# Kernel optimization log

Hardware: AMD Instinct MI355X
Metric: run time of the kernel (lower is better)

The kernel has to match this reference:

```python
import jax, jax.numpy as jnp
import numpy as np

HIDDEN = 512
EXP = 2048  # hidden * expansion_factor(4)

def _glorot(key, shape):
    fan_in = shape[0]
    return jax.random.normal(key, shape, dtype=jnp.float32) / np.sqrt(fan_in)

def setup_inputs() -> dict:
    key = jax.random.key(0)
    ks = jax.random.split(key, 6)
    B, S = 4, 4096
    return {
        "x": jax.random.normal(ks[0], (B, S, HIDDEN), dtype=jnp.float32),
        "W_in1": _glorot(ks[1], (HIDDEN, EXP)),
        "b_in1": jnp.zeros((EXP,), jnp.float32),
        "W_in2": _glorot(ks[2], (HIDDEN, EXP)),
        "b_in2": jnp.zeros((EXP,), jnp.float32),
        "W_z": _glorot(ks[3], (EXP, EXP)),
        "b_z": jnp.zeros((EXP,), jnp.float32),
        "W_h": _glorot(ks[4], (EXP, EXP)),
        "b_h": jnp.zeros((EXP,), jnp.float32),
        "W_out": _glorot(ks[5], (EXP, HIDDEN)),
        "b_out": jnp.zeros((HIDDEN,), jnp.float32),
    }

def _min_gru(x_in, W_z, b_z, W_h, b_h):
    # minGRU: h_t = (1 - z_t) * h_{t-1} + z_t * h_tilde_t, h_0 = 0
    z = jax.nn.sigmoid(jnp.einsum("bse,ef->bsf", x_in, W_z) + b_z)
    h_tilde = jnp.einsum("bse,ef->bsf", x_in, W_h) + b_h
    a = 1.0 - z          # decay coeff
    b = z * h_tilde      # input term
    def combine(c1, c2):
        a1, b1 = c1
        a2, b2 = c2
        return (a1 * a2, b1 * a2 + b2)
    _, h = jax.lax.associative_scan(combine, (a, b), axis=1)
    return h

def reference(x, W_in1, b_in1, W_in2, b_in2, W_z, b_z, W_h, b_h, W_out, b_out):
    x_in = jax.nn.silu(jnp.einsum("bsd,de->bse", x, W_in1) + b_in1)
    x_skip = jax.nn.silu(jnp.einsum("bsd,de->bse", x, W_in2) + b_in2)
    h = _min_gru(x_in, W_z, b_z, W_h, b_h)
    return jnp.einsum("bse,ed->bsd", x_skip + h, W_out) + b_out
```

## Files before the change

kernel.cpp:

```cpp
#include <hip/hip_runtime.h>
#include <hip/hip_bf16.h>


typedef __bf16 bf16x8 __attribute__((ext_vector_type(8)));
typedef __bf16 bf16x4 __attribute__((ext_vector_type(4)));
typedef float  f32x4  __attribute__((ext_vector_type(4)));

#define DEVINL __device__ __forceinline__

DEVINL void async_ld16(const __bf16* g, __bf16* l) {
    __builtin_amdgcn_global_load_lds(
        (const __attribute__((address_space(1))) void*)g,
        (__attribute__((address_space(3))) void*)l, 16, 0, 0);
}

DEVINL float fsigmoid(float v) { return 1.0f / (1.0f + __expf(-v)); }

template <int MODE>
__global__ __launch_bounds__(512, 4)
void gemm4(const __bf16* __restrict__ A, const __bf16* __restrict__ Bt,
           const float* __restrict__ bias, const float* __restrict__ bias2,
           void* __restrict__ out, void* __restrict__ out2, int N, int K,
           int bps, int seg_stride, int row_off)
{
    struct KL { __bf16 A[128 * 32]; __bf16 B[256 * 32]; };
    __shared__ union SM4 {
        KL kl[2];
        __bf16 ct[64 * 264];
    } sm;
    const int tid = threadIdx.x;
    const int bx = blockIdx.x;
    const int seg = bx / bps;
    const int within = bx - seg * bps;
    const int gm0 = row_off + seg * seg_stride + within * 128;
    const int om0 = bx * 128;
    const int n0 = blockIdx.y * 256;

    const int rA = tid >> 2,         kA = (tid & 3) ^ ((tid >> 3) & 3);
    const int c0 = tid, c1 = tid + 512;
    const int rB0 = c0 >> 2,         kB0 = (c0 & 3) ^ ((c0 >> 3) & 3);
    const int rB1 = c1 >> 2,         kB1 = (c1 & 3) ^ ((c1 >> 3) & 3);
    const __bf16* Ag  = A  + (size_t)(gm0 + rA)  * K + kA  * 8;
    const __bf16* Bg0 = Bt + (size_t)(n0 + rB0) * K + kB0 * 8;
    const __bf16* Bg1 = Bt + (size_t)(n0 + rB1) * K + kB1 * 8;

    const int lane = tid & 63;
    const int wave = tid >> 6;
    const int wm = wave >> 2;
    const int wn = wave & 3;
    const int quad = lane >> 4;
    const int r = lane & 15;
    const int swz = (quad ^ ((r >> 1) & 3)) * 8;

    f32x4 acc[4][4] = {};

    const int T = K >> 5;

    auto stage = [&](int t, int b) {
        const int kt = t << 5;
        async_ld16(Ag  + kt, sm.kl[b].A + tid * 8);
        async_ld16(Bg0 + kt, sm.kl[b].B + c0 * 8);
        async_ld16(Bg1 + kt, sm.kl[b].B + c1 * 8);
    };

    stage(0, 0);

    for (int t = 0; t < T; ++t) {
        const int cur = t & 1;
        if (t + 1 < T) {
            stage(t + 1, cur ^ 1);
            asm volatile("s_waitcnt vmcnt(3)\n\ts_barrier" ::: "memory");
        } else {
            asm volatile("s_waitcnt vmcnt(0)\n\ts_barrier" ::: "memory");
        }

        const __bf16* ap = sm.kl[cur].A + (wm * 64 + r) * 32 + swz;
        const __bf16* bp = sm.kl[cur].B + (wn * 64 + r) * 32 + swz;
        bf16x8 af[4], bf_[4];
#pragma unroll
        for (int m = 0; m < 4; ++m) af[m] = *(const bf16x8*)(ap + m * 512);
#pragma unroll
        for (int n = 0; n < 4; ++n) bf_[n] = *(const bf16x8*)(bp + n * 512);

        __builtin_amdgcn_s_setprio(1);
#pragma unroll
        for (int m = 0; m < 4; ++m)
#pragma unroll
            for (int n = 0; n < 4; ++n)
                acc[m][n] = __builtin_amdgcn_mfma_f32_16x16x32_bf16(
                    af[m], bf_[n], acc[m][n], 0, 0, 0);
        __builtin_amdgcn_s_setprio(0);

        asm volatile("s_waitcnt lgkmcnt(0)\n\ts_barrier" ::: "memory");
    }

    const bool lo = n0 < 2048;
    __bf16* dst = (__bf16*)out;
    const int cb = n0;
    const size_t stride = (size_t)N;
    float bvj[4];
#pragma unroll
    for (int nf = 0; nf < 4; ++nf) {
        const int gc = n0 + wn * 64 + nf * 16 + r;
        bvj[nf] = lo ? bias[gc] : bias2[gc - 2048];
    }

#pragma unroll
    for (int p = 0; p < 2; ++p) {
        if (wm == p) {
#pragma unroll
            for (int mm = 0; mm < 4; ++mm)
#pragma unroll
                for (int nf = 0; nf < 4; ++nf)
#pragma unroll
                    for (int k = 0; k < 4; ++k) {
                        const float v = acc[mm][nf][k] + bvj[nf];
                        sm.ct[(mm * 16 + quad * 4 + k) * 264 +
                              (wn * 64 + nf * 16 + r)] = (__bf16)v;
                    }
        }
        __syncthreads();
#pragma unroll
        for (int q = 0; q < 4; ++q) {
            const int chunk = q * 512 + tid;
            const int trow = chunk >> 5;
            const int tc = (chunk & 31) * 8;
            const bf16x8 vv = *(const bf16x8*)(sm.ct + trow * 264 + tc);
            *(bf16x8*)(dst + (size_t)(om0 + p * 64 + trow) * stride + cb + tc) = vv;
        }
        __syncthreads();
    }
}

struct KLoopSM { __bf16 A[2][128 * 32]; __bf16 B[2][128 * 32]; };

template <int MODE>
__global__ __launch_bounds__(256)
void gemm_bt(const __bf16* __restrict__ A, const __bf16* __restrict__ Bt,
             const float* __restrict__ bias, const float* __restrict__ bias2,
             void* __restrict__ out, void* __restrict__ out2, int N, int K,
             int bps, int seg_stride, int row_off)
{
    __shared__ union SM {
        KLoopSM kl;
        __bf16 ct[64 * 136];
        float  ctf[32 * 132];
    } sm;
    const int tid = threadIdx.x;
    const int bx = blockIdx.x;
    const int by = blockIdx.y;
    const int seg = bx / bps;
    const int within = bx - seg * bps;
    const int gm0 = row_off + seg * seg_stride + within * 128;
    const int om0 = bx * 128;
    const int n0 = by * 128;

    const int c0 = tid, c1 = tid + 256;
    const int r0 = c0 >> 2, k0 = (c0 & 3) ^ ((c0 >> 3) & 3);
    const int r1 = c1 >> 2, k1 = (c1 & 3) ^ ((c1 >> 3) & 3);
    const __bf16* Ag0 = A  + (size_t)(gm0 + r0) * K + k0 * 8;
    const __bf16* Ag1 = A  + (size_t)(gm0 + r1) * K + k1 * 8;
    const __bf16* Bg0 = Bt + (size_t)(n0 + r0) * K + k0 * 8;
    const __bf16* Bg1 = Bt + (size_t)(n0 + r1) * K + k1 * 8;

    const int lane = tid & 63;
    const int wave = tid >> 6;
    const int wrow = (wave >> 1) * 64;
    const int wcol = (wave & 1) * 64;
    const int quad = lane >> 4;
    const int r = lane & 15;
    const int swz = (quad ^ ((r >> 1) & 3)) * 8;

    f32x4 acc[4][4] = {};

    const int T = K >> 5;
    async_ld16(Ag0, sm.kl.A[0] + c0 * 8);
    async_ld16(Ag1, sm.kl.A[0] + c1 * 8);
    async_ld16(Bg0, sm.kl.B[0] + c0 * 8);
    async_ld16(Bg1, sm.kl.B[0] + c1 * 8);

    for (int t = 0; t < T; ++t) {
        const int cur = t & 1;
        if (t + 1 < T) {
            const int kt = (t + 1) << 5;
            async_ld16(Ag0 + kt, sm.kl.A[cur ^ 1] + c0 * 8);
            async_ld16(Ag1 + kt, sm.kl.A[cur ^ 1] + c1 * 8);
            async_ld16(Bg0 + kt, sm.kl.B[cur ^ 1] + c0 * 8);
            async_ld16(Bg1 + kt, sm.kl.B[cur ^ 1] + c1 * 8);
            asm volatile("s_waitcnt vmcnt(4)\n\ts_barrier" ::: "memory");
        } else {
            asm volatile("s_waitcnt vmcnt(0)\n\ts_barrier" ::: "memory");
        }

        const __bf16* ap = sm.kl.A[cur] + (wrow + r) * 32 + swz;
        const __bf16* bp = sm.kl.B[cur] + (wcol + r) * 32 + swz;
        bf16x8 af[4], bf_[4];
#pragma unroll
        for (int i = 0; i < 4; ++i) af[i] = *(const bf16x8*)(ap + i * 512);
#pragma unroll
        for (int i = 0; i < 4; ++i) bf_[i] = *(const bf16x8*)(bp + i * 512);
#pragma unroll
        for (int i = 0; i < 4; ++i)
#pragma unroll
            for (int j = 0; j < 4; ++j)
                acc[i][j] = __builtin_amdgcn_mfma_f32_16x16x32_bf16(
                    af[i], bf_[j], acc[i][j], 0, 0, 0);

        asm volatile("s_waitcnt lgkmcnt(0)\n\ts_barrier" ::: "memory");
    }

    if (MODE == 3) {
        float bvj[4];
#pragma unroll
        for (int j = 0; j < 4; ++j)
            bvj[j] = bias[n0 + wcol + j * 16 + r];
#pragma unroll
        for (int p = 0; p < 4; ++p) {
#pragma unroll
            for (int j = 0; j < 4; ++j)
#pragma unroll
                for (int k = 0; k < 4; ++k)
                    sm.ctf[((wave >> 1) * 16 + quad * 4 + k) * 132 +
                           (wcol + j * 16 + r)] = acc[p][j][k] + bvj[j];
            __syncthreads();
#pragma unroll
            for (int q = 0; q < 4; ++q) {
                const int chunk = q * 256 + tid;
                const int trow = chunk >> 5;
                const int tc4 = (chunk & 31) * 4;
                const f32x4 vv = *(const f32x4*)(sm.ctf + trow * 132 + tc4);
                const int grow = om0 + (trow >> 4) * 64 + p * 16 + (trow & 15);
                *(f32x4*)((float*)out + (size_t)grow * N + n0 + tc4) = vv;
            }
            __syncthreads();
        }
    } else {
        const bool lo = n0 < 2048;
        __bf16* dst;
        int cb;
        size_t stride;
        if (MODE == 0) {
            dst = lo ? (__bf16*)out : (__bf16*)out2;
            cb = lo ? n0 : n0 - 2048;
            stride = 2048;
        } else {
            dst = (__bf16*)out;
            cb = n0;
            stride = (size_t)N;
        }
        float bvj[4];
#pragma unroll
        for (int j = 0; j < 4; ++j) {
            const int gc = n0 + wcol + j * 16 + r;
            bvj[j] = lo ? bias[gc] : bias2[gc - 2048];
        }
#pragma unroll
        for (int p = 0; p < 2; ++p) {
#pragma unroll
            for (int ii = 0; ii < 2; ++ii) {
                const int i = 2 * p + ii;
#pragma unroll
                for (int j = 0; j < 4; ++j)
#pragma unroll
                    for (int k = 0; k < 4; ++k) {
                        const float v = acc[i][j][k] + bvj[j];
                        const __bf16 o = (MODE == 0) ? (__bf16)(v * fsigmoid(v))
                                                     : (__bf16)v;
                        sm.ct[((wave >> 1) * 32 + ii * 16 + quad * 4 + k) * 136 +
                              (wcol + j * 16 + r)] = o;
                    }
            }
            __syncthreads();
#pragma unroll
            for (int q = 0; q < 4; ++q) {
                const int chunk = q * 256 + tid;
                const int trow = chunk >> 4;
                const int tc = (chunk & 15) * 8;
                const bf16x8 vv = *(const bf16x8*)(sm.ct + trow * 136 + tc);
                const int grow = om0 + (trow >> 5) * 64 + p * 32 + (trow & 31);
                *(bf16x8*)(dst + (size_t)grow * stride + cb + tc) = vv;
            }
            __syncthreads();
        }
    }
}

#define SSEG 32
#define SCOLS 32
__global__ __launch_bounds__(1024)
void scan_kernel(const __bf16* __restrict__ raw, __bf16* __restrict__ xskip,
                 float* __restrict__ carry, int CS, int S, int t0, int first)
{
    __shared__ float Als[SSEG][SCOLS];
    __shared__ float Bls[SSEG][SCOLS];
    const int lane = threadIdx.x & (SCOLS - 1);
    const int w = threadIdx.x >> 5;
    const int nb8 = gridDim.x >> 3;
    const int lin = (blockIdx.x & 7) * nb8 + (blockIdx.x >> 3);
    const int gpb = 2048 / SCOLS;
    const int batch = lin / gpb;
    const int col = (lin - batch * gpb) * SCOLS + lane;
    const int L = CS / SSEG;
    const int tbeg = w * L;

    const size_t rbase = ((size_t)batch * CS + tbeg) * 4096 + col;

    float av[32], bv[32];
    float A = 1.0f, Bv = 0.0f;
    {
        size_t idx = rbase;
#pragma unroll
        for (int t = 0; t < 32; ++t, idx += 4096) {
            const float z = fsigmoid((float)raw[idx]);
            const float b = z * (float)raw[idx + 2048];
            const float a = 1.0f - z;
            av[t] = a;
            bv[t] = b;
            Bv = a * Bv + b;
            A *= a;
        }
    }
    Als[w][lane] = A;
    Bls[w][lane] = Bv;
    __syncthreads();

    const int ch = batch * 2048 + col;
    float h = first ? 0.0f : carry[ch];
    for (int s = 0; s < w; ++s)
        h = Als[s][lane] * h + Bls[s][lane];
    if (w == SSEG - 1)
        carry[ch] = A * h + Bv;

    {
        size_t gidx = ((size_t)batch * S + t0 + tbeg) * 2048 + col;
#pragma unroll
        for (int t = 0; t < 32; ++t, gidx += 2048) {
            h = av[t] * h + bv[t];
            xskip[gidx] = (__bf16)((float)xskip[gidx] + h);
        }
    }
}

__global__ __launch_bounds__(256)
void conv_f32_bf16(const float* __restrict__ x, __bf16* __restrict__ y, int n4)
{
    const int i = blockIdx.x * 256 + threadIdx.x;
    if (i >= n4) return;
    const float4 v = ((const float4*)x)[i];
    bf16x4 o;
    o[0] = (__bf16)v.x; o[1] = (__bf16)v.y; o[2] = (__bf16)v.z; o[3] = (__bf16)v.w;
    ((bf16x4*)y)[i] = o;
}

__global__ __launch_bounds__(256)
void transpose_bf16(const float* __restrict__ W, __bf16* __restrict__ Wt, int K, int N)
{
    __shared__ float tile[32][33];
    const int tx = threadIdx.x & 31;
    const int ty = threadIdx.x >> 5;
    const int nb = blockIdx.x * 32;
    const int kb = blockIdx.y * 32;
#pragma unroll
    for (int i = 0; i < 32; i += 8)
        tile[ty + i][tx] = W[(size_t)(kb + ty + i) * N + nb + tx];
    __syncthreads();
#pragma unroll
    for (int i = 0; i < 32; i += 8)
        Wt[(size_t)(nb + ty + i) * K + kb + tx] = (__bf16)tile[tx][ty + i];
}

extern "C" void kernel_launch(void* const* d_in, const int* in_sizes, int n_in,
                              void* d_out, int out_size, void* d_ws, size_t ws_size,
                              hipStream_t stream)
{
    const float* x     = (const float*)d_in[0];
    const float* W_in1 = (const float*)d_in[1];
    const float* b_in1 = (const float*)d_in[2];
    const float* W_in2 = (const float*)d_in[3];
    const float* b_in2 = (const float*)d_in[4];
    const float* W_z   = (const float*)d_in[5];
    const float* b_z   = (const float*)d_in[6];
    const float* W_h   = (const float*)d_in[7];
    const float* b_h   = (const float*)d_in[8];
    const float* W_out = (const float*)d_in[9];
    const float* b_out = (const float*)d_in[10];

    const int B = 4, S = 4096, H = 512, E = 2048;
    const int M = B * S;
    const int CS = 1024;
    const int NC = S / CS;
    const int MC = B * CS;

    const size_t MiB = 1024 * 1024;
    const size_t NEEDED = 183 * MiB;
    if (ws_size < NEEDED) return;

    char* ws = (char*)d_ws;
    __bf16* xb    = (__bf16*)(ws + 0);
    __bf16* rawzh = (__bf16*)(ws + 0);
    float*  carry = (float*) (ws + 32 * MiB);
    __bf16* xin   = (__bf16*)(ws + 33 * MiB);
    __bf16* xskip = (__bf16*)(ws + 97 * MiB);
    __bf16* Wt12  = (__bf16*)(ws + 161 * MiB);
    __bf16* Wtzh  = (__bf16*)(ws + 165 * MiB);
    __bf16* Wto   = (__bf16*)(ws + 181 * MiB);

    conv_f32_bf16<<<(M * H / 4 + 255) / 256, 256, 0, stream>>>(x, xb, M * H / 4);
    transpose_bf16<<<dim3(E / 32, H / 32), 256, 0, stream>>>(W_in1, Wt12, H, E);
    transpose_bf16<<<dim3(E / 32, H / 32), 256, 0, stream>>>(W_in2, Wt12 + (size_t)E * H, H, E);
    transpose_bf16<<<dim3(E / 32, E / 32), 256, 0, stream>>>(W_z, Wtzh, E, E);
    transpose_bf16<<<dim3(E / 32, E / 32), 256, 0, stream>>>(W_h, Wtzh + (size_t)E * E, E, E);
    transpose_bf16<<<dim3(H / 32, E / 32), 256, 0, stream>>>(W_out, Wto, E, H);

    gemm_bt<0><<<dim3(M / 128, 2 * E / 128), 256, 0, stream>>>(
        xb, Wt12, b_in1, b_in2, xin, xskip, 2 * E, H, M / 128, 0, 0);

    for (int c = 0; c < NC; ++c) {
        const int row_off = c * CS;
        gemm4<4><<<dim3(MC / 128, 2 * E / 256), 512, 0, stream>>>(
            xin, Wtzh, b_z, b_h, rawzh, nullptr, 2 * E, E, CS / 128, S, row_off);
        scan_kernel<<<(B * E) / SCOLS, 1024, 0, stream>>>(
            rawzh, xskip, carry, CS, S, row_off, c == 0);
    }

    gemm_bt<3><<<dim3(M / 128, H / 128), 256, 0, stream>>>(
        xskip, Wto, b_out, nullptr, (float*)d_out, nullptr, H, E, M / 128, 0, 0);
}
```

Before: 652.5 us.

## Enlarge z/h GEMM tile to 256x256 with 64-deep K steps

Replaces the 128x256 tile, K=32 z/h projection GEMM with a 256x256 tile that stages 64 K-elements per step. It uses an 8-way XOR swizzle for the wider LDS rows, and each wave now accumulates 8x4 MFMA fragments. This raises arithmetic intensity per LDS load, halves the number of barrier-separated K iterations, and halves the block count. In exchange, LDS use grows to about 128KB for the double buffer, register pressure doubles and occupancy drops to 2 blocks per CU. The chunked grid may also underfill the GPU.

```diff
diff --git a/kernel.cpp b/kernel.cpp
--- a/kernel.cpp
+++ b/kernel.cpp
@@ -17,14 +17,14 @@
 DEVINL float fsigmoid(float v) { return 1.0f / (1.0f + __expf(-v)); }
 
 template <int MODE>
-__global__ __launch_bounds__(512, 4)
-void gemm4(const __bf16* __restrict__ A, const __bf16* __restrict__ Bt,
-           const float* __restrict__ bias, const float* __restrict__ bias2,
-           void* __restrict__ out, void* __restrict__ out2, int N, int K,
-           int bps, int seg_stride, int row_off)
-{
-    struct KL { __bf16 A[128 * 32]; __bf16 B[256 * 32]; };
-    __shared__ union SM4 {
+__global__ __launch_bounds__(512, 2)
+void gemm3k(const __bf16* __restrict__ A, const __bf16* __restrict__ Bt,
+            const float* __restrict__ bias, const float* __restrict__ bias2,
+            void* __restrict__ out, void* __restrict__ out2, int N, int K,
+            int bps, int seg_stride, int row_off)
+{
+    struct KL { __bf16 A[256 * 64]; __bf16 B[256 * 64]; };
+    __shared__ union SM3K {
         KL kl[2];
         __bf16 ct[64 * 264];
     } sm;
@@ -32,17 +32,24 @@
     const int bx = blockIdx.x;
     const int seg = bx / bps;
     const int within = bx - seg * bps;
-    const int gm0 = row_off + seg * seg_stride + within * 128;
-    const int om0 = bx * 128;
+    const int gm0 = row_off + seg * seg_stride + within * 256;
+    const int om0 = bx * 256;
     const int n0 = blockIdx.y * 256;
 
-    const int rA = tid >> 2,         kA = (tid & 3) ^ ((tid >> 3) & 3);
-    const int c0 = tid, c1 = tid + 512;
-    const int rB0 = c0 >> 2,         kB0 = (c0 & 3) ^ ((c0 >> 3) & 3);
-    const int rB1 = c1 >> 2,         kB1 = (c1 & 3) ^ ((c1 >> 3) & 3);
-    const __bf16* Ag  = A  + (size_t)(gm0 + rA)  * K + kA  * 8;
-    const __bf16* Bg0 = Bt + (size_t)(n0 + rB0) * K + kB0 * 8;
-    const __bf16* Bg1 = Bt + (size_t)(n0 + rB1) * K + kB1 * 8;
+    int rA[4], kA[4];
+#pragma unroll
+    for (int j = 0; j < 4; ++j) {
+        const int s = tid + 512 * j;
+        rA[j] = s >> 3;
+        kA[j] = (s & 7) ^ (rA[j] & 7);
+    }
+    const __bf16* Agp[4];
+    const __bf16* Bgp[4];
+#pragma unroll
+    for (int j = 0; j < 4; ++j) {
+        Agp[j] = A  + (size_t)(gm0 + rA[j]) * K + kA[j] * 8;
+        Bgp[j] = Bt + (size_t)(n0 + rA[j]) * K + kA[j] * 8;
+    }
 
     const int lane = tid & 63;
     const int wave = tid >> 6;
@@ -50,49 +57,63 @@
     const int wn = wave & 3;
     const int quad = lane >> 4;
     const int r = lane & 15;
-    const int swz = (quad ^ ((r >> 1) & 3)) * 8;
-
-    f32x4 acc[4][4] = {};
-
-    const int T = K >> 5;
+
+    f32x4 acc[8][4] = {};
+
+    const int T = K >> 6;
 
     auto stage = [&](int t, int b) {
-        const int kt = t << 5;
-        async_ld16(Ag  + kt, sm.kl[b].A + tid * 8);
-        async_ld16(Bg0 + kt, sm.kl[b].B + c0 * 8);
-        async_ld16(Bg1 + kt, sm.kl[b].B + c1 * 8);
+        const int kt = t << 6;
+#pragma unroll
+        for (int j = 0; j < 4; ++j)
+            async_ld16(Agp[j] + kt, sm.kl[b].A + (tid + 512 * j) * 8);
+#pragma unroll
+        for (int j = 0; j < 4; ++j)
+            async_ld16(Bgp[j] + kt, sm.kl[b].B + (tid + 512 * j) * 8);
     };
 
     stage(0, 0);
+
+    const int swz0 = ((0 * 4 + quad) ^ (r & 7)) * 8;
+    const int swz1 = ((1 * 4 + quad) ^ (r & 7)) * 8;
 
     for (int t = 0; t < T; ++t) {
         const int cur = t & 1;
         if (t + 1 < T) {
             stage(t + 1, cur ^ 1);
-            asm volatile("s_waitcnt vmcnt(3)\n\ts_barrier" ::: "memory");
+            asm volatile("s_waitcnt vmcnt(8)\n\ts_barrier" ::: "memory");
         } else {
             asm volatile("s_waitcnt vmcnt(0)\n\ts_barrier" ::: "memory");
         }
 
-        const __bf16* ap = sm.kl[cur].A + (wm * 64 + r) * 32 + swz;
-        const __bf16* bp = sm.kl[cur].B + (wn * 64 + r) * 32 + swz;
-        bf16x8 af[4], bf_[4];
-#pragma unroll
-        for (int m = 0; m < 4; ++m) af[m] = *(const bf16x8*)(ap + m * 512);
-#pragma unroll
-        for (int n = 0; n < 4; ++n) bf_[n] = *(const bf16x8*)(bp + n * 512);
-
-        __builtin_amdgcn_s_setprio(1);
-#pragma unroll
-        for (int m = 0; m < 4; ++m)
+        const __bf16* apb = sm.kl[cur].A + (wm * 128 + r) * 64;
+        const __bf16* bpb = sm.kl[cur].B + (wn * 64 + r) * 64;
+
+#pragma unroll
+        for (int ks = 0; ks < 2; ++ks) {
+            const int swz = ks ? swz1 : swz0;
+            bf16x8 af[8], bf_[4];
+#pragma unroll
+            for (int m = 0; m < 8; ++m)
+                af[m] = *(const bf16x8*)(apb + m * 1024 + swz);
 #pragma unroll
             for (int n = 0; n < 4; ++n)
-                acc[m][n] = __builtin_amdgcn_mfma_f32_16x16x32_bf16(
-                    af[m], bf_[n], acc[m][n], 0, 0, 0);
-        __builtin_amdgcn_s_setprio(0);
+                bf_[n] = *(const bf16x8*)(bpb + n * 1024 + swz);
+
+            __builtin_amdgcn_s_setprio(1);
+#pragma unroll
+            for (int m = 0; m < 8; ++m)
+#pragma unroll
+                for (int n = 0; n < 4; ++n)
+                    acc[m][n] = __builtin_amdgcn_mfma_f32_16x16x32_bf16(
+                        af[m], bf_[n], acc[m][n], 0, 0, 0);
+            __builtin_amdgcn_s_setprio(0);
+        }
 
         asm volatile("s_waitcnt lgkmcnt(0)\n\ts_barrier" ::: "memory");
     }
+
+    __syncthreads();
 
     const bool lo = n0 < 2048;
     __bf16* dst = (__bf16*)out;
@@ -106,15 +127,16 @@
     }
 
 #pragma unroll
-    for (int p = 0; p < 2; ++p) {
-        if (wm == p) {
+    for (int p = 0; p < 4; ++p) {
+        if (wm == (p >> 1)) {
+            const int mb = (p & 1) * 4;
 #pragma unroll
             for (int mm = 0; mm < 4; ++mm)
 #pragma unroll
                 for (int nf = 0; nf < 4; ++nf)
 #pragma unroll
                     for (int k = 0; k < 4; ++k) {
-                        const float v = acc[mm][nf][k] + bvj[nf];
+                        const float v = acc[mb + mm][nf][k] + bvj[nf];
                         sm.ct[(mm * 16 + quad * 4 + k) * 264 +
                               (wn * 64 + nf * 16 + r)] = (__bf16)v;
                     }
@@ -417,8 +439,8 @@
 
     for (int c = 0; c < NC; ++c) {
         const int row_off = c * CS;
-        gemm4<4><<<dim3(MC / 128, 2 * E / 256), 512, 0, stream>>>(
-            xin, Wtzh, b_z, b_h, rawzh, nullptr, 2 * E, E, CS / 128, S, row_off);
+        gemm3k<4><<<dim3(MC / 256, 2 * E / 256), 512, 0, stream>>>(
+            xin, Wtzh, b_z, b_h, rawzh, nullptr, 2 * E, E, CS / 256, S, row_off);
         scan_kernel<<<(B * E) / SCOLS, 1024, 0, stream>>>(
             rawzh, xskip, carry, CS, S, row_off, c == 0);
     }
```

After: 615.3 us. 1.06x faster.
